# Kernel optimization log

Hardware: AMD Instinct MI355X
Metric: run time of the kernel (lower is better)

The kernel has to match this reference:

```python
import jax, jax.numpy as jnp
import numpy as np


def setup_inputs() -> dict:
    key = jax.random.key(0)
    k0, k1, k2 = jax.random.split(key, 3)
    B, C, n, k, cout = 32, 256, 32, 3, 256
    x = jax.random.normal(k0, (B, C, n, n), jnp.float32)
    weight = jax.random.normal(k1, (C, C, k, k), jnp.float32) * 0.05
    H = jax.random.normal(k2, (cout, C, 1, 1), jnp.float32) / np.sqrt(C)
    bias = jnp.zeros((cout,), jnp.float32)
    alpha = jnp.ones((1,), jnp.float32)  # module inits alpha = ||wfft||, so alpha/||wfft|| scaling = wfft itself when alpha matches; treated as a learned scalar param
    return {"x": x, "weight": weight, "alpha": alpha, "H": H, "bias": bias}


def reference(x, weight, alpha, H, bias):
    B, C, n, _ = x.shape
    k = weight.shape[-1]
    s = (k - 1) // 2
    nf = n // 2 + 1
    F = n * nf

    # fft_shift_matrix(n, -s)[:, :n//2+1] : exp(-1j*2*pi*s*(i+j)/n)
    idx = jnp.arange(n)
    phase = (idx[:, None] + idx[None, :]).astype(jnp.float32)
    shift = jnp.exp(1j * (2.0 * np.pi * (-s) / n) * phase)[:, :nf].reshape(F, 1, 1)

    # x -> frequency domain, (F, C, B)
    xfft = jnp.fft.rfft2(x).transpose(2, 3, 1, 0).reshape(F, C, B)

    # weight -> frequency domain, (F, C, C), conjugated and phase-shifted
    wfft = shift * jnp.conj(jnp.fft.rfft2(weight, s=(n, n)).reshape(C, C, F).transpose(2, 0, 1))

    # Cayley transform (ED=True) per frequency: Q = (I + A)^{-1} (I - A), A = W - W^H
    W = (alpha / jnp.linalg.norm(wfft)) * wfft
    A = W - jnp.conj(jnp.swapaxes(W, 1, 2))
    I = jnp.eye(C, dtype=W.dtype)
    Q = jnp.linalg.solve(I + A, I - A)  # (F, C, C) batched complex solve

    # apply orthogonal filter in frequency domain and transform back
    wx = Q @ xfft                                   # (F, C, B)
    yfft = wx.reshape(n, nf, C, B).transpose(3, 2, 0, 1)  # (B, C, n, nf)
    y = jnp.fft.irfft2(yfft)                        # (B, C, n, n)

    # 1x1 conv with H (cout, C, 1, 1) + bias
    y = jnp.einsum("bchw,oc->bohw", y, H[:, :, 0, 0]) + bias[:, None, None]
    return y
```

## Files before the change

kernel.cpp:

```cpp
#include <hip/hip_runtime.h>
#include <hip/hip_fp8.h>
#include <cstddef>

#define PI_F 3.14159265358979323846f

#define NCH 256
#define NB  32
#define NF  544

#define ASCALE     65536.0f
#define INV_ASCALE (1.0f/65536.0f)

typedef short  bf16x8 __attribute__((ext_vector_type(8)));
typedef float  f32x4  __attribute__((ext_vector_type(4)));

#define SZ_AFRAG ((size_t)NF*8*16*1024)
#define SZ_P8    ((size_t)NF*NB*NCH)
#define SZ_PB    ((size_t)NF*NB*NCH*2)
#define SZ_P32   ((size_t)NF*NB*NCH*4)
#define OFF_AFRAG ((size_t)0)
#define OFF_T8R  (OFF_AFRAG + SZ_AFRAG)
#define OFF_T8I  (OFF_T8R + SZ_P8)
#define OFF_Z8R  (OFF_T8I + SZ_P8)
#define OFF_Z8I  (OFF_Z8R + SZ_P8)
#define OFF_Z32R (OFF_Z8I + SZ_P8)
#define OFF_Z32I (OFF_Z32R + SZ_P32)
#define OFF_WXHR (OFF_Z32I + SZ_P32)
#define OFF_WXHI (OFF_WXHR + SZ_PB)
#define OFF_HFRAG (OFF_WXHI + SZ_PB)
#define SZ_HFRAG ((size_t)8*16*1024)
#define OFF_RED  (OFF_HFRAG + SZ_HFRAG)
#define WS_NEED  (OFF_RED + (size_t)4096)

__device__ constexpr float COS32[32] = {
     1.0000000000f,  0.9807852804f,  0.9238795325f,  0.8314696123f,
     0.7071067812f,  0.5555702330f,  0.3826834324f,  0.1950903220f,
     0.0000000000f, -0.1950903220f, -0.3826834324f, -0.5555702330f,
    -0.7071067812f, -0.8314696123f, -0.9238795325f, -0.9807852804f,
    -1.0000000000f, -0.9807852804f, -0.9238795325f, -0.8314696123f,
    -0.7071067812f, -0.5555702330f, -0.3826834324f, -0.1950903220f,
    -0.0000000000f,  0.1950903220f,  0.3826834324f,  0.5555702330f,
     0.7071067812f,  0.8314696123f,  0.9238795325f,  0.9807852804f };
__device__ constexpr float SIN32[32] = {
     0.0000000000f,  0.1950903220f,  0.3826834324f,  0.5555702330f,
     0.7071067812f,  0.8314696123f,  0.9238795325f,  0.9807852804f,
     1.0000000000f,  0.9807852804f,  0.9238795325f,  0.8314696123f,
     0.7071067812f,  0.5555702330f,  0.3826834324f,  0.1950903220f,
     0.0000000000f, -0.1950903220f, -0.3826834324f, -0.5555702330f,
    -0.7071067812f, -0.8314696123f, -0.9238795325f, -0.9807852804f,
    -1.0000000000f, -0.9807852804f, -0.9238795325f, -0.8314696123f,
    -0.7071067812f, -0.5555702330f, -0.3826834324f, -0.1950903220f };

__device__ __forceinline__ unsigned short f2bf(float x) {
    unsigned int u = __float_as_uint(x);
    u += 0x7FFFu + ((u >> 16) & 1u);
    return (unsigned short)(u >> 16);
}
__device__ __forceinline__ float bf2f(unsigned int h) {
    return __uint_as_float(h << 16);
}
__device__ __forceinline__ unsigned int pack2(float a, float b) {
    return (unsigned int)f2bf(a) | ((unsigned int)f2bf(b) << 16);
}
__device__ __forceinline__ unsigned char f2e4m3(float x) {
    __hip_fp8_e4m3 h(x);
    return (unsigned char)h.__x;
}
__device__ __forceinline__ float e4m3f(unsigned int b) {
    __hip_fp8_e4m3 h; h.__x = (__hip_fp8_storage_t)b;
    return (float)h;
}
__device__ __forceinline__ unsigned int pk4_e4m3(const float* v) {
    return (unsigned)f2e4m3(v[0]) | ((unsigned)f2e4m3(v[1]) << 8) |
           ((unsigned)f2e4m3(v[2]) << 16) | ((unsigned)f2e4m3(v[3]) << 24);
}

__global__ void norm_part(const float* __restrict__ w, float* __restrict__ red) {
    int idx = blockIdx.x * 256 + threadIdx.x;
    const float* wp = w + (size_t)idx * 9;
    float s2 = 0.f, aa = 0.f, bb = 0.f;
#pragma unroll
    for (int u = 0; u < 3; u++) {
        float w0 = wp[u*3+0], w1 = wp[u*3+1], w2 = wp[u*3+2];
        s2 += w0*w0 + w1*w1 + w2*w2;
        float au = w0 + w1 + w2, bu = w0 - w1 + w2;
        aa += au*au; bb += bu*bu;
    }
    float p = 512.f*s2 + 16.f*(aa + bb);
    __shared__ float sm[256];
    sm[threadIdx.x] = p; __syncthreads();
    for (int s = 128; s > 0; s >>= 1) {
        if (threadIdx.x < s) sm[threadIdx.x] += sm[threadIdx.x + s];
        __syncthreads();
    }
    if (threadIdx.x == 0) red[blockIdx.x] = sm[0];
}

__global__ void norm_final(const float* __restrict__ red, const float* __restrict__ alpha,
                           float* __restrict__ sig) {
    __shared__ float sm[256];
    sm[threadIdx.x] = red[threadIdx.x]; __syncthreads();
    for (int s = 128; s > 0; s >>= 1) {
        if (threadIdx.x < s) sm[threadIdx.x] += sm[threadIdx.x + s];
        __syncthreads();
    }
    if (threadIdx.x == 0) sig[0] = alpha[0] / sqrtf(sm[0]);
}

__global__ void hfrag_build(const float* __restrict__ H, unsigned short* __restrict__ Hfrag) {
    int kk = blockIdx.x, mt = blockIdx.y, lane = threadIdx.x;
    int o = mt*16 + (lane & 15), c0 = kk*32 + (lane >> 4)*8;
    const float* hp = H + (size_t)o*NCH + c0;
    uint4 u;
    u.x = pack2(hp[0], hp[1]); u.y = pack2(hp[2], hp[3]);
    u.z = pack2(hp[4], hp[5]); u.w = pack2(hp[6], hp[7]);
    ((uint4*)Hfrag)[((size_t)kk*16 + mt)*64 + lane] = u;
}

__global__ __launch_bounds__(256) void rfft2_reg(const float* __restrict__ x,
                                                 float2* __restrict__ tmp)
{
    __shared__ float2 T[8][544];
    __shared__ float wc[32], wsn[32];
    int t = threadIdx.x;
    int half = t >> 5, lane = t & 31;
    int cb = blockIdx.x * 8 + half;
    int c = cb >> 5, b = cb & 31;
    if (t < 32) { wc[t] = COS32[t]; wsn[t] = SIN32[t]; }
    float xr[32];
    const float* xp = x + ((size_t)(b * NCH + c)) * 1024 + lane * 32;
#pragma unroll
    for (int q = 0; q < 8; q++) {
        float4 v = *(const float4*)(xp + q*4);
        xr[q*4+0] = v.x; xr[q*4+1] = v.y; xr[q*4+2] = v.z; xr[q*4+3] = v.w;
    }
    float x0v = xr[0], x16v = xr[16];
    float es[15], os[15];
#pragma unroll
    for (int s = 1; s <= 15; s++) { es[s-1] = xr[s] + xr[32-s]; os[s-1] = xr[s] - xr[32-s]; }
#pragma unroll
    for (int j = 0; j < 17; j++) {
        float ax = x0v + ((j & 1) ? -x16v : x16v);
        float ay = 0.f;
#pragma unroll
        for (int s = 1; s <= 15; s++) {
            int m = (j * s) & 31;
            ax += es[s-1] * COS32[m];
            ay -= os[s-1] * SIN32[m];
        }
        T[half][lane*17 + j] = make_float2(ax, ay);
    }
    __syncthreads();
    float wr_[16], wi_[16];
#pragma unroll
    for (int r = 0; r < 16; r++) {
        int m = (lane * r) & 31;
        wr_[r] = wc[m]; wi_[r] = wsn[m];
    }
    float sgn = (lane & 1) ? -1.f : 1.f;
    float2* op = tmp + (size_t)cb * 544 + lane * 17;
#pragma unroll
    for (int j = 0; j < 17; j++) {
        float ax = 0.f, ay = 0.f;
#pragma unroll
        for (int r = 0; r < 16; r++) {
            float2 t1 = T[half][r*17 + j];
            float2 t2 = T[half][(r+16)*17 + j];
            float ex = fmaf(sgn, t2.x, t1.x);
            float ey = fmaf(sgn, t2.y, t1.y);
            ax += ex * wr_[r] + ey * wi_[r];
            ay += ey * wr_[r] - ex * wi_[r];
        }
        op[j] = make_float2(ax, ay);
    }
}

__global__ __launch_bounds__(256) void transpose_z(const float2* __restrict__ tmp,
        float* __restrict__ z32r, float* __restrict__ z32i,
        unsigned char* __restrict__ z8r, unsigned char* __restrict__ z8i)
{
    __shared__ float2 tile[32][33];
    int ct = blockIdx.x, ft = blockIdx.y, b = blockIdx.z;
    int t = threadIdx.x;
#pragma unroll
    for (int it = 0; it < 4; it++) {
        int idx = t + it*256; int cl = idx >> 5, fl = idx & 31;
        tile[cl][fl] = tmp[((size_t)((ct*32 + cl)*32 + b))*544 + ft*32 + fl];
    }
    __syncthreads();
#pragma unroll
    for (int it = 0; it < 4; it++) {
        int idx = t + it*256; int fl = idx >> 5, cl = idx & 31;
        float2 v = tile[cl][fl];
        size_t zi_ = ((size_t)(ft*32 + fl)*NB + b)*NCH + ct*32 + cl;
        z32r[zi_] = v.x; z32i[zi_] = v.y;
        z8r[zi_] = f2e4m3(v.x); z8i[zi_] = f2e4m3(v.y);
    }
}

__global__ __launch_bounds__(256) void a_build_direct(const float* __restrict__ w,
        const float* __restrict__ sig, unsigned int* __restrict__ Afrag)
{
    int mt = blockIdx.x, kk = blockIdx.y, j = blockIdx.z;
    int t = threadIdx.x;
    int wv = t & 127;
    int c   = mt*16 + ((wv >> 1) & 15);
    int cp0 = kk*32 + (wv >> 5)*8 + (wv & 1)*4;
    bool isReal = (t < 128);
    float sS = sig[0] * ASCALE;
    float sgnS = isReal ? sS : -sS;
    f32x4 P1, P2, P3, P4, P5;
#pragma unroll
    for (int e = 0; e < 4; e++) {
        int cp = cp0 + e;
        const float* p1 = w + ((size_t)c*NCH + cp)*9;
        const float* p2 = w + ((size_t)cp*NCH + c)*9;
        float u_[9];
#pragma unroll
        for (int q = 0; q < 9; q++)
            u_[q] = isReal ? (p1[q] - p2[q]) : (p1[q] + p2[q]);
        if (isReal) {
            P1[e] = sgnS * u_[4];
            P2[e] = sgnS * (u_[3] + u_[5]);
            P3[e] = sgnS * (u_[1] + u_[7]);
            P4[e] = sgnS * (u_[0] + u_[2] + u_[6] + u_[8]);
            P5[e] = sgnS * ((u_[6] - u_[8]) - (u_[0] - u_[2]));
        } else {
            P1[e] = sgnS * (u_[3] - u_[5]);
            P2[e] = sgnS * ((u_[0] - u_[2]) + (u_[6] - u_[8]));
            P3[e] = sgnS * (u_[1] - u_[7]);
            P4[e] = sgnS * ((u_[0] + u_[2]) - (u_[6] + u_[8]));
            P5[e] = 0.f;
        }
    }
    float cps = COS32[j], sns = SIN32[j];
    f32x4 Aj, Bj, Cj;
    if (isReal) { Aj = P1 + cps*P2; Bj = P3 + cps*P4; Cj = sns*P5; }
    else        { Aj = sns*P1;      Bj = sns*P2;      Cj = P3 + cps*P4; }
    unsigned int* out = Afrag + ((size_t)j*128 + kk*16 + mt)*256 + t;
#pragma unroll
    for (int i = 0; i < 32; i++) {
        f32x4 v = Aj + COS32[i]*Bj + SIN32[i]*Cj;
        *out = (unsigned)f2e4m3(v[0]) | ((unsigned)f2e4m3(v[1]) << 8)
             | ((unsigned)f2e4m3(v[2]) << 16) | ((unsigned)f2e4m3(v[3]) << 24);
        out += (size_t)17*32768;
    }
}

__global__ __launch_bounds__(256) void neum1(
    const unsigned char* __restrict__ Afrag,
    const unsigned char* __restrict__ z8r, const unsigned char* __restrict__ z8i,
    unsigned char* __restrict__ outR, unsigned char* __restrict__ outI)
{
    __shared__ uint2 lz8[2][1024];
    int fl = blockIdx.x >> 1, half = blockIdx.x & 1;
    int f = fl;
    int t = threadIdx.x;
    const uint2* s0 = (const uint2*)(z8r + (size_t)f*8192);
    const uint2* s1 = (const uint2*)(z8i + (size_t)f*8192);
    for (int u = t; u < 2048; u += 256) {
        int p = u >> 10, idx = u & 1023;
        int b = idx >> 5, o16 = idx & 31;
        lz8[p][b*32 + (o16 ^ (b & 7))] = (p ? s1 : s0)[idx];
    }
    __syncthreads();
    int w = t >> 6, lane = t & 63, lo = lane & 15, hi = lane >> 4;
    f32x4 accr[2][2], acci[2][2];
    f32x4 zz = {0.f, 0.f, 0.f, 0.f};
#pragma unroll
    for (int mt = 0; mt < 2; mt++)
#pragma unroll
        for (int nt = 0; nt < 2; nt++) { accr[mt][nt] = zz; acci[mt][nt] = zz; }
    const uint2* A8 = (const uint2*)Afrag;
    for (int kk = 0; kk < 8; kk++) {
        long ar[2], ai[2], ain[2];
#pragma unroll
        for (int mt = 0; mt < 2; mt++) {
            int mtg = half*8 + w*2 + mt;
            size_t idx = (((size_t)fl*8 + kk)*16 + mtg)*128 + lane;
            uint2 va = A8[idx], vb = A8[idx + 64];
            ar[mt] = __builtin_bit_cast(long, va);
            ai[mt] = __builtin_bit_cast(long, vb);
            uint2 vn = make_uint2(vb.x ^ 0x80808080u, vb.y ^ 0x80808080u);
            ain[mt] = __builtin_bit_cast(long, vn);
        }
        long zr[2], zi_[2];
#pragma unroll
        for (int nt = 0; nt < 2; nt++) {
            int b = nt*16 + lo;
            int du = b*32 + ((kk*4 + hi) ^ (b & 7));
            zr[nt]  = __builtin_bit_cast(long, lz8[0][du]);
            zi_[nt] = __builtin_bit_cast(long, lz8[1][du]);
        }
#pragma unroll
        for (int mt = 0; mt < 2; mt++)
#pragma unroll
            for (int nt = 0; nt < 2; nt++) {
                accr[mt][nt] = __builtin_amdgcn_mfma_f32_16x16x32_fp8_fp8(ar[mt],  zr[nt],  accr[mt][nt], 0, 0, 0);
                accr[mt][nt] = __builtin_amdgcn_mfma_f32_16x16x32_fp8_fp8(ain[mt], zi_[nt], accr[mt][nt], 0, 0, 0);
                acci[mt][nt] = __builtin_amdgcn_mfma_f32_16x16x32_fp8_fp8(ar[mt],  zi_[nt], acci[mt][nt], 0, 0, 0);
                acci[mt][nt] = __builtin_amdgcn_mfma_f32_16x16x32_fp8_fp8(ai[mt],  zr[nt],  acci[mt][nt], 0, 0, 0);
            }
    }
#pragma unroll
    for (int mt = 0; mt < 2; mt++)
#pragma unroll
        for (int nt = 0; nt < 2; nt++) {
            int c0 = half*128 + w*32 + mt*16 + hi*4;
            int b  = nt*16 + lo;
            int duc = b*32 + (((c0 & 255) >> 3) ^ (b & 7));
            int sel = (c0 >> 2) & 1;
            uint2 q0 = lz8[0][duc], q1 = lz8[1][duc];
            unsigned qr = sel ? q0.y : q0.x;
            unsigned qi = sel ? q1.y : q1.x;
            float zfr[4] = { e4m3f(qr & 0xffu), e4m3f((qr>>8)&0xffu),
                             e4m3f((qr>>16)&0xffu), e4m3f(qr>>24) };
            float zfi[4] = { e4m3f(qi & 0xffu), e4m3f((qi>>8)&0xffu),
                             e4m3f((qi>>16)&0xffu), e4m3f(qi>>24) };
            size_t zb = ((size_t)f*NB + b)*NCH + c0;
            float vr[4], vi[4];
#pragma unroll
            for (int jj = 0; jj < 4; jj++) {
                vr[jj] = zfr[jj] - accr[mt][nt][jj] * INV_ASCALE;
                vi[jj] = zfi[jj] - acci[mt][nt][jj] * INV_ASCALE;
            }
            *(unsigned int*)(outR + zb) = pk4_e4m3(vr);
            *(unsigned int*)(outI + zb) = pk4_e4m3(vi);
        }
}

__global__ __launch_bounds__(512) void neum2h(
    const unsigned char* __restrict__ Afrag,
    const unsigned short* __restrict__ Hfrag,
    const unsigned char* __restrict__ TR, const unsigned char* __restrict__ TI,
    const float* __restrict__ z32r, const float* __restrict__ z32i,
    unsigned short* __restrict__ wxhR, unsigned short* __restrict__ wxhI)
{
    __shared__ uint2 lz8[2][1024];
    __shared__ uint4 lw[2][1024];
    int fl = blockIdx.x;
    int f = fl;
    int t = threadIdx.x;
    const uint2* s0 = (const uint2*)(TR + (size_t)f*8192);
    const uint2* s1 = (const uint2*)(TI + (size_t)f*8192);
    for (int u = t; u < 2048; u += 512) {
        int p = u >> 10, idx = u & 1023;
        int b = idx >> 5, o16 = idx & 31;
        lz8[p][b*32 + (o16 ^ (b & 7))] = (p ? s1 : s0)[idx];
    }
    __syncthreads();
    int w = t >> 6, lane = t & 63, lo = lane & 15, hi = lane >> 4;
    const uint2* A8 = (const uint2*)Afrag;
    const uint4* H4 = (const uint4*)Hfrag;
    f32x4 accr[2][2], acci[2][2];
    f32x4 zz = {0.f, 0.f, 0.f, 0.f};
#pragma unroll
    for (int mt = 0; mt < 2; mt++)
#pragma unroll
        for (int nt = 0; nt < 2; nt++) { accr[mt][nt] = zz; acci[mt][nt] = zz; }
    for (int kk = 0; kk < 8; kk++) {
        long ar[2], ai[2], ain[2];
#pragma unroll
        for (int mt = 0; mt < 2; mt++) {
            int mtg = w*2 + mt;
            size_t idx = (((size_t)fl*8 + kk)*16 + mtg)*128 + lane;
            uint2 va = A8[idx], vb = A8[idx + 64];
            ar[mt] = __builtin_bit_cast(long, va);
            ai[mt] = __builtin_bit_cast(long, vb);
            uint2 vn = make_uint2(vb.x ^ 0x80808080u, vb.y ^ 0x80808080u);
            ain[mt] = __builtin_bit_cast(long, vn);
        }
        long zr[2], zi_[2];
#pragma unroll
        for (int nt = 0; nt < 2; nt++) {
            int b = nt*16 + lo;
            int du = b*32 + ((kk*4 + hi) ^ (b & 7));
            zr[nt]  = __builtin_bit_cast(long, lz8[0][du]);
            zi_[nt] = __builtin_bit_cast(long, lz8[1][du]);
        }
#pragma unroll
        for (int mt = 0; mt < 2; mt++)
#pragma unroll
            for (int nt = 0; nt < 2; nt++) {
                accr[mt][nt] = __builtin_amdgcn_mfma_f32_16x16x32_fp8_fp8(ar[mt],  zr[nt],  accr[mt][nt], 0, 0, 0);
                accr[mt][nt] = __builtin_amdgcn_mfma_f32_16x16x32_fp8_fp8(ain[mt], zi_[nt], accr[mt][nt], 0, 0, 0);
                acci[mt][nt] = __builtin_amdgcn_mfma_f32_16x16x32_fp8_fp8(ar[mt],  zi_[nt], acci[mt][nt], 0, 0, 0);
                acci[mt][nt] = __builtin_amdgcn_mfma_f32_16x16x32_fp8_fp8(ai[mt],  zr[nt],  acci[mt][nt], 0, 0, 0);
            }
    }
    __syncthreads();
#pragma unroll
    for (int mt = 0; mt < 2; mt++)
#pragma unroll
        for (int nt = 0; nt < 2; nt++) {
            int c0 = w*32 + mt*16 + hi*4;
            int b  = nt*16 + lo;
            size_t zb = ((size_t)f*NB + b)*NCH + c0;
            float4 z4r = *(const float4*)(z32r + zb);
            float4 z4i = *(const float4*)(z32i + zb);
            const float k2 = 2.f * INV_ASCALE;
            float vr[4] = { z4r.x - k2*accr[mt][nt][0], z4r.y - k2*accr[mt][nt][1],
                            z4r.z - k2*accr[mt][nt][2], z4r.w - k2*accr[mt][nt][3] };
            float vi[4] = { z4i.x - k2*acci[mt][nt][0], z4i.y - k2*acci[mt][nt][1],
                            z4i.z - k2*acci[mt][nt][2], z4i.w - k2*acci[mt][nt][3] };
            int o16c = c0 >> 3;
            int duc = b*32 + (o16c ^ (b & 7));
            int sel = (c0 >> 2) & 1;
            ((uint2*)&lw[0][duc])[sel] = make_uint2(pack2(vr[0], vr[1]), pack2(vr[2], vr[3]));
            ((uint2*)&lw[1][duc])[sel] = make_uint2(pack2(vi[0], vi[1]), pack2(vi[2], vi[3]));
        }
    __syncthreads();
#pragma unroll
    for (int mt = 0; mt < 2; mt++)
#pragma unroll
        for (int nt = 0; nt < 2; nt++) { accr[mt][nt] = zz; acci[mt][nt] = zz; }
    for (int kk = 0; kk < 8; kk++) {
        bf16x8 hm[2];
#pragma unroll
        for (int mt = 0; mt < 2; mt++) {
            int mtg = w*2 + mt;
            hm[mt] = __builtin_bit_cast(bf16x8, H4[((size_t)kk*16 + mtg)*64 + lane]);
        }
        bf16x8 zr[2], zi_[2];
#pragma unroll
        for (int nt = 0; nt < 2; nt++) {
            int b = nt*16 + lo;
            int du = b*32 + ((kk*4 + hi) ^ (b & 7));
            zr[nt]  = __builtin_bit_cast(bf16x8, lw[0][du]);
            zi_[nt] = __builtin_bit_cast(bf16x8, lw[1][du]);
        }
#pragma unroll
        for (int mt = 0; mt < 2; mt++)
#pragma unroll
            for (int nt = 0; nt < 2; nt++) {
                accr[mt][nt] = __builtin_amdgcn_mfma_f32_16x16x32_bf16(hm[mt], zr[nt],  accr[mt][nt], 0, 0, 0);
                acci[mt][nt] = __builtin_amdgcn_mfma_f32_16x16x32_bf16(hm[mt], zi_[nt], acci[mt][nt], 0, 0, 0);
            }
    }
#pragma unroll
    for (int mt = 0; mt < 2; mt++)
#pragma unroll
        for (int nt = 0; nt < 2; nt++) {
            int o0 = w*32 + mt*16 + hi*4;
            int b  = nt*16 + lo;
            size_t zb = ((size_t)f*NB + b)*NCH + o0;
            *(uint2*)(wxhR + zb) = make_uint2(pack2(accr[mt][nt][0], accr[mt][nt][1]),
                                              pack2(accr[mt][nt][2], accr[mt][nt][3]));
            *(uint2*)(wxhI + zb) = make_uint2(pack2(acci[mt][nt][0], acci[mt][nt][1]),
                                              pack2(acci[mt][nt][2], acci[mt][nt][3]));
        }
}

template<int RH>
__device__ __forceinline__ void ifft_i_body(const unsigned short* __restrict__ YR,
                                            const unsigned short* __restrict__ YI,
                                            float2* __restrict__ G, int j, int ob)
{
    float2 Gacc[16];
#pragma unroll
    for (int rr = 0; rr < 16; rr++) Gacc[rr] = make_float2(0.f, 0.f);
#pragma unroll
    for (int i = 0; i < 32; i++) {
        size_t yi_ = (size_t)(i * 17 + j) * 8192 + ob;
        float Yx = bf2f(YR[yi_]);
        float Yy = bf2f(YI[yi_]);
#pragma unroll
        for (int rr = 0; rr < 16; rr++) {
            int m = (i * (RH * 16 + rr)) & 31;
            Gacc[rr].x += Yx*COS32[m] - Yy*SIN32[m];
            Gacc[rr].y += Yx*SIN32[m] + Yy*COS32[m];
        }
    }
#pragma unroll
    for (int rr = 0; rr < 16; rr++) {
        G[((size_t)(j*32 + RH*16 + rr))*8192 + ob] =
            make_float2(Gacc[rr].x * (1.f/32.f), Gacc[rr].y * (1.f/32.f));
    }
}

__global__ __launch_bounds__(256) void ifft_i(const unsigned short* __restrict__ YR,
                                              const unsigned short* __restrict__ YI,
                                              float2* __restrict__ G) {
    int bid = blockIdx.x;
    int j   = bid >> 6;
    int rh  = (bid >> 5) & 1;
    int obc = bid & 31;
    int ob  = obc * 256 + threadIdx.x;
    if (rh == 0) ifft_i_body<0>(YR, YI, G, j, ob);
    else         ifft_i_body<1>(YR, YI, G, j, ob);
}

__global__ __launch_bounds__(256) void irfft_j(const float2* __restrict__ G,
                                               const float* __restrict__ bias,
                                               float* __restrict__ out) {
    int gid = blockIdx.x * 256 + threadIdx.x;
    int r = gid >> 13, ob = gid & 8191;
    int b = ob >> 8, o = ob & 255;
    float2 Gv[17];
#pragma unroll
    for (int jj = 0; jj < 17; jj++)
        Gv[jj] = G[((size_t)(jj*32 + r))*8192 + ob];
    float y[32];
    float g0 = Gv[0].x, g16 = Gv[16].x;
#pragma unroll
    for (int s = 0; s < 32; s++) y[s] = g0 + ((s & 1) ? -g16 : g16);
#pragma unroll
    for (int jj = 1; jj < 16; jj++) {
#pragma unroll
        for (int s = 0; s < 32; s++) {
            int m = (jj * s) & 31;
            y[s] += 2.f * (Gv[jj].x * COS32[m] - Gv[jj].y * SIN32[m]);
        }
    }
    float bv = bias[o];
    float* op = out + ((size_t)(b * NCH + o) * 32 + r) * 32;
#pragma unroll
    for (int s = 0; s < 32; s++) op[s] = y[s] * (1.f/32.f) + bv;
}

extern "C" void kernel_launch(void* const* d_in, const int* in_sizes, int n_in,
                              void* d_out, int out_size, void* d_ws, size_t ws_size,
                              hipStream_t stream) {
    (void)in_sizes; (void)n_in; (void)out_size;
    if (ws_size < WS_NEED) return;

    const float* x     = (const float*)d_in[0];
    const float* w     = (const float*)d_in[1];
    const float* alpha = (const float*)d_in[2];
    const float* H     = (const float*)d_in[3];
    const float* bias  = (const float*)d_in[4];
    float* out = (float*)d_out;

    char* ws = (char*)d_ws;
    unsigned char* Afrag = (unsigned char*)(ws + OFF_AFRAG);
    float2* tmp = (float2*)(ws + OFF_AFRAG);
    float2* G   = (float2*)(ws + OFF_AFRAG);
    unsigned char* t8r  = (unsigned char*)(ws + OFF_T8R);
    unsigned char* t8i  = (unsigned char*)(ws + OFF_T8I);
    unsigned char* z8r  = (unsigned char*)(ws + OFF_Z8R);
    unsigned char* z8i  = (unsigned char*)(ws + OFF_Z8I);
    float* z32r = (float*)(ws + OFF_Z32R);
    float* z32i = (float*)(ws + OFF_Z32I);
    unsigned short* wxhR = (unsigned short*)(ws + OFF_WXHR);
    unsigned short* wxhI = (unsigned short*)(ws + OFF_WXHI);
    unsigned short* Hfrag = (unsigned short*)(ws + OFF_HFRAG);
    float* red = (float*)(ws + OFF_RED);
    float* sig = red + 256;

    norm_part<<<256, 256, 0, stream>>>(w, red);
    norm_final<<<1, 256, 0, stream>>>(red, alpha, sig);
    hfrag_build<<<dim3(8, 16), 64, 0, stream>>>(H, Hfrag);

    rfft2_reg<<<1024, 256, 0, stream>>>(x, tmp);
    transpose_z<<<dim3(8, 17, 32), 256, 0, stream>>>(tmp, z32r, z32i, z8r, z8i);

    a_build_direct<<<dim3(16, 8, 17), 256, 0, stream>>>(w, sig, (unsigned int*)Afrag);
    neum1<<<NF*2, 256, 0, stream>>>(Afrag, z8r, z8i, t8r, t8i);
    neum2h<<<NF, 512, 0, stream>>>(Afrag, Hfrag, t8r, t8i, z32r, z32i, wxhR, wxhI);

    ifft_i<<<1088, 256, 0, stream>>>(wxhR, wxhI, G);
    irfft_j<<<1024, 256, 0, stream>>>(G, bias, out);
}
```

Before: 182.0 us.

## Fuse two Neumann-series kernels into one, keeping intermediate in LDS

Merges neum1 and neum2h into a single 512-thread kernel per frequency. The first-iteration result is written back into shared memory instead of global fp8 buffers, which removes one launch and a global round trip of the intermediate. In exchange each block does twice the first-stage work with fewer blocks (544 instead of 1088), which may lower parallelism in that stage. It also stages rfft2 output through shared memory so the global stores are coalesced.

```diff
diff --git a/kernel.cpp b/kernel.cpp
--- a/kernel.cpp
+++ b/kernel.cpp
@@ -19,9 +19,7 @@
 #define SZ_PB    ((size_t)NF*NB*NCH*2)
 #define SZ_P32   ((size_t)NF*NB*NCH*4)
 #define OFF_AFRAG ((size_t)0)
-#define OFF_T8R  (OFF_AFRAG + SZ_AFRAG)
-#define OFF_T8I  (OFF_T8R + SZ_P8)
-#define OFF_Z8R  (OFF_T8I + SZ_P8)
+#define OFF_Z8R  (OFF_AFRAG + SZ_AFRAG)
 #define OFF_Z8I  (OFF_Z8R + SZ_P8)
 #define OFF_Z32R (OFF_Z8I + SZ_P8)
 #define OFF_Z32I (OFF_Z32R + SZ_P32)
@@ -121,6 +119,7 @@
                                                  float2* __restrict__ tmp)
 {
     __shared__ float2 T[8][544];
+    __shared__ float2 Z[8][544];
     __shared__ float wc[32], wsn[32];
     int t = threadIdx.x;
     int half = t >> 5, lane = t & 31;
@@ -158,7 +157,6 @@
         wr_[r] = wc[m]; wi_[r] = wsn[m];
     }
     float sgn = (lane & 1) ? -1.f : 1.f;
-    float2* op = tmp + (size_t)cb * 544 + lane * 17;
 #pragma unroll
     for (int j = 0; j < 17; j++) {
         float ax = 0.f, ay = 0.f;
@@ -171,8 +169,14 @@
             ax += ex * wr_[r] + ey * wi_[r];
             ay += ey * wr_[r] - ex * wi_[r];
         }
-        op[j] = make_float2(ax, ay);
-    }
+        Z[half][lane*17 + j] = make_float2(ax, ay);
+    }
+    __syncthreads();
+    float2* outp = tmp + (size_t)blockIdx.x * 8 * 544;
+    const float2* zf = (const float2*)Z;
+#pragma unroll
+    for (int u = 0; u < 17; u++)
+        outp[u*256 + t] = zf[u*256 + t];
 }
 
 __global__ __launch_bounds__(256) void transpose_z(const float2* __restrict__ tmp,
@@ -247,36 +251,40 @@
     }
 }
 
-__global__ __launch_bounds__(256) void neum1(
+__global__ __launch_bounds__(512) void neum_fused(
     const unsigned char* __restrict__ Afrag,
+    const unsigned short* __restrict__ Hfrag,
     const unsigned char* __restrict__ z8r, const unsigned char* __restrict__ z8i,
-    unsigned char* __restrict__ outR, unsigned char* __restrict__ outI)
+    const float* __restrict__ z32r, const float* __restrict__ z32i,
+    unsigned short* __restrict__ wxhR, unsigned short* __restrict__ wxhI)
 {
     __shared__ uint2 lz8[2][1024];
-    int fl = blockIdx.x >> 1, half = blockIdx.x & 1;
+    __shared__ uint4 lw[2][1024];
+    int fl = blockIdx.x;
     int f = fl;
     int t = threadIdx.x;
     const uint2* s0 = (const uint2*)(z8r + (size_t)f*8192);
     const uint2* s1 = (const uint2*)(z8i + (size_t)f*8192);
-    for (int u = t; u < 2048; u += 256) {
+    for (int u = t; u < 2048; u += 512) {
         int p = u >> 10, idx = u & 1023;
         int b = idx >> 5, o16 = idx & 31;
         lz8[p][b*32 + (o16 ^ (b & 7))] = (p ? s1 : s0)[idx];
     }
     __syncthreads();
     int w = t >> 6, lane = t & 63, lo = lane & 15, hi = lane >> 4;
+    const uint2* A8 = (const uint2*)Afrag;
+    const uint4* H4 = (const uint4*)Hfrag;
     f32x4 accr[2][2], acci[2][2];
     f32x4 zz = {0.f, 0.f, 0.f, 0.f};
 #pragma unroll
     for (int mt = 0; mt < 2; mt++)
 #pragma unroll
         for (int nt = 0; nt < 2; nt++) { accr[mt][nt] = zz; acci[mt][nt] = zz; }
-    const uint2* A8 = (const uint2*)Afrag;
     for (int kk = 0; kk < 8; kk++) {
         long ar[2], ai[2], ain[2];
 #pragma unroll
         for (int mt = 0; mt < 2; mt++) {
-            int mtg = half*8 + w*2 + mt;
+            int mtg = w*2 + mt;
             size_t idx = (((size_t)fl*8 + kk)*16 + mtg)*128 + lane;
             uint2 va = A8[idx], vb = A8[idx + 64];
             ar[mt] = __builtin_bit_cast(long, va);
@@ -302,13 +310,14 @@
                 acci[mt][nt] = __builtin_amdgcn_mfma_f32_16x16x32_fp8_fp8(ai[mt],  zr[nt],  acci[mt][nt], 0, 0, 0);
             }
     }
+    __syncthreads();
 #pragma unroll
     for (int mt = 0; mt < 2; mt++)
 #pragma unroll
         for (int nt = 0; nt < 2; nt++) {
-            int c0 = half*128 + w*32 + mt*16 + hi*4;
+            int c0 = w*32 + mt*16 + hi*4;
             int b  = nt*16 + lo;
-            int duc = b*32 + (((c0 & 255) >> 3) ^ (b & 7));
+            int duc = b*32 + ((c0 >> 3) ^ (b & 7));
             int sel = (c0 >> 2) & 1;
             uint2 q0 = lz8[0][duc], q1 = lz8[1][duc];
             unsigned qr = sel ? q0.y : q0.x;
@@ -317,43 +326,16 @@
                              e4m3f((qr>>16)&0xffu), e4m3f(qr>>24) };
             float zfi[4] = { e4m3f(qi & 0xffu), e4m3f((qi>>8)&0xffu),
                              e4m3f((qi>>16)&0xffu), e4m3f(qi>>24) };
-            size_t zb = ((size_t)f*NB + b)*NCH + c0;
             float vr[4], vi[4];
 #pragma unroll
             for (int jj = 0; jj < 4; jj++) {
                 vr[jj] = zfr[jj] - accr[mt][nt][jj] * INV_ASCALE;
                 vi[jj] = zfi[jj] - acci[mt][nt][jj] * INV_ASCALE;
             }
-            *(unsigned int*)(outR + zb) = pk4_e4m3(vr);
-            *(unsigned int*)(outI + zb) = pk4_e4m3(vi);
-        }
-}
-
-__global__ __launch_bounds__(512) void neum2h(
-    const unsigned char* __restrict__ Afrag,
-    const unsigned short* __restrict__ Hfrag,
-    const unsigned char* __restrict__ TR, const unsigned char* __restrict__ TI,
-    const float* __restrict__ z32r, const float* __restrict__ z32i,
-    unsigned short* __restrict__ wxhR, unsigned short* __restrict__ wxhI)
-{
-    __shared__ uint2 lz8[2][1024];
-    __shared__ uint4 lw[2][1024];
-    int fl = blockIdx.x;
-    int f = fl;
-    int t = threadIdx.x;
-    const uint2* s0 = (const uint2*)(TR + (size_t)f*8192);
-    const uint2* s1 = (const uint2*)(TI + (size_t)f*8192);
-    for (int u = t; u < 2048; u += 512) {
-        int p = u >> 10, idx = u & 1023;
-        int b = idx >> 5, o16 = idx & 31;
-        lz8[p][b*32 + (o16 ^ (b & 7))] = (p ? s1 : s0)[idx];
-    }
-    __syncthreads();
-    int w = t >> 6, lane = t & 63, lo = lane & 15, hi = lane >> 4;
-    const uint2* A8 = (const uint2*)Afrag;
-    const uint4* H4 = (const uint4*)Hfrag;
-    f32x4 accr[2][2], acci[2][2];
-    f32x4 zz = {0.f, 0.f, 0.f, 0.f};
+            ((unsigned int*)&lz8[0][duc])[sel] = pk4_e4m3(vr);
+            ((unsigned int*)&lz8[1][duc])[sel] = pk4_e4m3(vi);
+        }
+    __syncthreads();
 #pragma unroll
     for (int mt = 0; mt < 2; mt++)
 #pragma unroll
@@ -535,8 +517,6 @@
     unsigned char* Afrag = (unsigned char*)(ws + OFF_AFRAG);
     float2* tmp = (float2*)(ws + OFF_AFRAG);
     float2* G   = (float2*)(ws + OFF_AFRAG);
-    unsigned char* t8r  = (unsigned char*)(ws + OFF_T8R);
-    unsigned char* t8i  = (unsigned char*)(ws + OFF_T8I);
     unsigned char* z8r  = (unsigned char*)(ws + OFF_Z8R);
     unsigned char* z8i  = (unsigned char*)(ws + OFF_Z8I);
     float* z32r = (float*)(ws + OFF_Z32R);
@@ -555,8 +535,7 @@
     transpose_z<<<dim3(8, 17, 32), 256, 0, stream>>>(tmp, z32r, z32i, z8r, z8i);
 
     a_build_direct<<<dim3(16, 8, 17), 256, 0, stream>>>(w, sig, (unsigned int*)Afrag);
-    neum1<<<NF*2, 256, 0, stream>>>(Afrag, z8r, z8i, t8r, t8i);
-    neum2h<<<NF, 512, 0, stream>>>(Afrag, Hfrag, t8r, t8i, z32r, z32i, wxhR, wxhI);
+    neum_fused<<<NF, 512, 0, stream>>>(Afrag, Hfrag, z8r, z8i, z32r, z32i, wxhR, wxhI);
 
     ifft_i<<<1088, 256, 0, stream>>>(wxhR, wxhI, G);
     irfft_j<<<1024, 256, 0, stream>>>(G, bias, out);
```

Result: faster. 172.5 us (-5.2%).
